# Performance work log

Hardware: AMD Instinct MI355X
Metric: run time of the kernel (lower is better)

The kernel has to match this reference:

```python
import jax, jax.numpy as jnp
import numpy as np
import math

L_DEG, N_PTS, T_ER, P_RAD, C_IN, C_OUT = 4, 8192, 15, 5, 16, 16


def _cg(j1, m1, j2, m2, j3, m3):
    # Clebsch-Gordan coefficient <j1 m1 j2 m2 | j3 m3> (Racah formula),
    # replacing sympy's CG(...).doit() used by the original module.
    if m1 + m2 != m3:
        return 0.0
    if j3 < abs(j1 - j2) or j3 > j1 + j2:
        return 0.0
    f = math.factorial
    pre = math.sqrt((2 * j3 + 1) * f(j3 + j1 - j2) * f(j3 - j1 + j2) * f(j1 + j2 - j3) / f(j1 + j2 + j3 + 1))
    pre *= math.sqrt(f(j3 + m3) * f(j3 - m3) * f(j1 - m1) * f(j1 + m1) * f(j2 - m2) * f(j2 + m2))
    s = 0.0
    for k in range(max(0, j2 - j3 - m1, j1 - j3 + m2), min(j1 + j2 - j3, j1 - m1, j2 + m2) + 1):
        s += (-1.0) ** k / (f(k) * f(j1 + j2 - j3 - k) * f(j1 - m1 - k) * f(j2 + m2 - k) * f(j3 - j2 + m1 + k) * f(j3 - j1 - m2 + k))
    return pre * s


def _precompute(L):
    # Mirrors PrecomputingTensorsForConv6D.
    tens, coefs = [], []
    for l in range(L):
        for l1 in range(L):
            for l2 in range(abs(l - l1), min(L, l + l1 + 1)):
                coefs.append(8.0 * np.pi ** 2 / (2 * l1 + 1)
                             * np.sqrt((2 * l + 1) * (2 * l1 + 1) / (4.0 * np.pi * (2 * l2 + 1)))
                             * _cg(l, 0, l1, 0, l2, 0))
                T1 = np.zeros((l + 1, l1 + 1, l2 + 1), np.float32)
                T2 = np.zeros_like(T1)
                T3 = np.zeros_like(T1)
                for k in range(l + 1):
                    for k1 in range(l1 + 1):
                        if k + k1 < l2 + 1:
                            T1[k, k1, k + k1] = _cg(l, k, l1, k1, l2, k + k1) * (-1) ** k1
                        if k1 > 0 and abs(k - k1) < l2 + 1:
                            if k - k1 >= 0:
                                T2[k, k1, k - k1] = _cg(l, k, l1, -k1, l2, k - k1) * (-1) ** l1
                            else:
                                T3[k, k1, k1 - k] = (-1) ** (k1 - k) * (-1) ** (l1 + l2) * _cg(l, k, l1, -k1, l2, k - k1)
                tens += [T1, T2, T3]
    return tens, [float(c) for c in coefs]


_TENS_NP, _COEFS = _precompute(L_DEG)
_TENS = [jnp.asarray(t, jnp.float32) for t in _TENS_NP]


def _forward(xs, ws, bs):
    L = L_DEG
    # zero the imaginary k=0 rows, as done via temp_term in build()
    ws_m = list(ws)
    bs_m = list(bs)
    for l in range(L):
        mk = (jnp.arange(l + 1) > 0).astype(jnp.float32)
        ws_m[2 * l + 1] = ws[2 * l + 1] * mk[:, None, None, None, None]
        bs_m[2 * l + 1] = bs[2 * l + 1] * mk[None, :, None, None]
    out = []
    itr = 0
    for l in range(L):
        o_r = 0.0
        o_i = 0.0
        for l1 in range(L):
            wr, wi = ws_m[2 * l1], ws_m[2 * l1 + 1]
            for l2 in range(abs(l - l1), min(L, l + l1 + 1)):
                c = _COEFS[itr]
                T1, T2, T3 = _TENS[3 * itr], _TENS[3 * itr + 1], _TENS[3 * itr + 2]
                xr, xi = xs[2 * l2], xs[2 * l2 + 1]
                # x: [n, t, k(l2+1), p, i]; w: [m(l1+1), t, p, i, j]; T: [l(l+1), m, k]
                o_r = o_r + c * jnp.einsum('lmk,ntkpi,mtpij->nlpj', T1 + T2 + T3, xr, wr) \
                          - c * jnp.einsum('lmk,ntkpi,mtpij->nlpj', T1 - T2 + T3, xi, wi)
                o_i = o_i + c * jnp.einsum('lmk,ntkpi,mtpij->nlpj', T1 - T2 - T3, xr, wi) \
                          + c * jnp.einsum('lmk,ntkpi,mtpij->nlpj', T1 + T2 - T3, xi, wr)
                itr += 1
        out.append(o_r + bs_m[2 * l])
        out.append(o_i + bs_m[2 * l + 1])
    return tuple(out)


def setup_inputs() -> dict:
    key = jax.random.key(0)
    ks = jax.random.split(key, 24)
    inp = {}
    i = 0
    for l in range(L_DEG):
        for part in ('r', 'i'):
            inp['x%d%s' % (l, part)] = jax.random.normal(ks[i], (N_PTS, T_ER, l + 1, P_RAD, C_IN), jnp.float32)
            i += 1
    for l in range(L_DEG):
        for part in ('r', 'i'):
            inp['w%d%s' % (l, part)] = jax.random.normal(ks[i], (l + 1, T_ER, P_RAD, C_IN, C_OUT), jnp.float32) * 0.05
            i += 1
    for l in range(L_DEG):
        for part in ('r', 'i'):
            inp['b%d%s' % (l, part)] = jax.random.normal(ks[i], (1, l + 1, P_RAD, C_OUT), jnp.float32) * 0.05
            i += 1
    return inp


def reference(x0r, x0i, x1r, x1i, x2r, x2i, x3r, x3i,
              w0r, w0i, w1r, w1i, w2r, w2i, w3r, w3i,
              b0r, b0i, b1r, b1i, b2r, b2i, b3r, b3i):
    xs = [x0r, x0i, x1r, x1i, x2r, x2i, x3r, x3i]
    ws = [w0r, w0i, w1r, w1i, w2r, w2i, w3r, w3i]
    bs = [b0r, b0i, b1r, b1i, b2r, b2i, b3r, b3i]
    return _forward(xs, ws, bs)
```

## Files before the change

kernel.cpp:

```cpp
#include <hip/hip_runtime.h>

#define PI_D 3.14159265358979323846


typedef __attribute__((ext_vector_type(8))) short short8;
typedef __attribute__((ext_vector_type(4))) float f32x4;

struct Ptrs8 { const float* p[8]; };

__device__ __forceinline__ ushort f2bf(float x){
  uint u = __float_as_uint(x);
  return (ushort)((u + 0x7fffu + ((u>>16)&1u)) >> 16);
}

__device__ __forceinline__ double dfact(int n){ double r=1.0; for(int i=2;i<=n;++i) r*=(double)i; return r; }

__device__ double cg_coef(int j1,int m1,int j2,int m2,int j3,int m3){
  if(m1+m2!=m3) return 0.0;
  if(j3<abs(j1-j2)||j3>j1+j2) return 0.0;
  if(abs(m1)>j1||abs(m2)>j2||abs(m3)>j3) return 0.0;
  double pre = sqrt((2.0*j3+1.0)*dfact(j3+j1-j2)*dfact(j3-j1+j2)*dfact(j1+j2-j3)/dfact(j1+j2+j3+1));
  pre *= sqrt(dfact(j3+m3)*dfact(j3-m3)*dfact(j1-m1)*dfact(j1+m1)*dfact(j2-m2)*dfact(j2+m2));
  int kmin = max(0,max(j2-j3-m1,j1-j3+m2));
  int kmax = min(j1+j2-j3,min(j1-m1,j2+m2));
  double s=0.0;
  for(int k=kmin;k<=kmax;++k){
    double d = dfact(k)*dfact(j1+j2-j3-k)*dfact(j1-m1-k)*dfact(j2+m2-k)*dfact(j3-j2+m1+k)*dfact(j3-j1-m2+k);
    s += ((k&1)?-1.0:1.0)/d;
  }
  return pre*s;
}

__device__ __forceinline__ int gidx(int l,int l2,int combo,int lr,int kx,int l1,int m){
  return ((((((l*4+l2)*4+combo)*4+lr)*4+kx)*4+l1)*4+m);
}

__global__ void g_kernel(float* __restrict__ G){
  int tid = threadIdx.x;
  for(int e=tid;e<16384;e+=blockDim.x) G[e]=0.0f;
  __syncthreads();
  int trip = tid >> 4;
  int sub  = tid & 15;
  int lr = sub >> 2, m = sub & 3;
  int idx=0;
  for(int l=0;l<4;l++)for(int l1=0;l1<4;l1++){
    int lo=abs(l-l1), hi=min(3,l+l1);
    for(int l2=lo;l2<=hi;l2++){
      if(idx==trip && lr<=l && m<=l1){
        double c = 8.0*PI_D*PI_D/(2.0*l1+1.0)
                 * sqrt((2.0*l+1.0)*(2.0*l1+1.0)/(4.0*PI_D*(2.0*l2+1.0)))
                 * cg_coef(l,0,l1,0,l2,0);
        if(lr+m<=l2){
          float f = (float)(c * cg_coef(l,lr,l1,m,l2,lr+m) * ((m&1)?-1.0:1.0));
          G[gidx(l,l2,0,lr,lr+m,l1,m)] += f;
          G[gidx(l,l2,1,lr,lr+m,l1,m)] -= f;
          G[gidx(l,l2,2,lr,lr+m,l1,m)] += f;
          G[gidx(l,l2,3,lr,lr+m,l1,m)] += f;
        }
        if(m>0 && abs(lr-m)<=l2){
          if(lr-m>=0){
            float f = (float)(c * cg_coef(l,lr,l1,-m,l2,lr-m) * ((l1&1)?-1.0:1.0));
            G[gidx(l,l2,0,lr,lr-m,l1,m)] += f;
            G[gidx(l,l2,1,lr,lr-m,l1,m)] += f;
            G[gidx(l,l2,2,lr,lr-m,l1,m)] -= f;
            G[gidx(l,l2,3,lr,lr-m,l1,m)] += f;
          } else {
            float f = (float)(c * (((m-lr)&1)?-1.0:1.0) * (((l1+l2)&1)?-1.0:1.0)
                              * cg_coef(l,lr,l1,-m,l2,lr-m));
            G[gidx(l,l2,0,lr,m-lr,l1,m)] += f;
            G[gidx(l,l2,1,lr,m-lr,l1,m)] -= f;
            G[gidx(l,l2,2,lr,m-lr,l1,m)] -= f;
            G[gidx(l,l2,3,lr,m-lr,l1,m)] -= f;
          }
        }
      }
      idx++;
    }
  }
}

__device__ __forceinline__ void decode_kb(int kb,int& l2,int& partp,int& kx,int& t){
  int kbo;
  if(kb<30){l2=0;kbo=0;} else if(kb<90){l2=1;kbo=30;} else if(kb<180){l2=2;kbo=90;} else {l2=3;kbo=180;}
  int rem = kb-kbo;
  int per = (l2+1)*15;
  partp = rem/per;
  int q = rem%per;
  kx = q/15; t = q%15;
}

__device__ __forceinline__ void decode_col(int col,int& l,int& part,int& lr,int& j){
  int co;
  if(col<32){l=0;co=0;} else if(col<96){l=1;co=32;} else if(col<192){l=2;co=96;} else {l=3;co=192;}
  int cr = col-co; int per=(l+1)*16;
  part = cr/per; int q = cr%per; lr = q>>4; j = q&15;
}

__global__ void w2_kernel(const float* __restrict__ G, Ptrs8 wp, ushort* __restrict__ W2){
  long e = (long)blockIdx.x*256 + threadIdx.x;
  if(e >= 7680000L) return;
  int b8 = (int)(e & 7);
  int ln = (int)((e>>3) & 63);
  int ks = (int)((e>>9) & 1);
  int kt = (int)((e>>10) % 75);
  long rr = (e>>10) / 75;
  int cw = (int)(rr % 20);
  int p  = (int)(rr / 20);
  int col = cw*16 + (ln&15);
  int K = kt*64 + ks*32 + ((ln>>4)<<3) + b8;
  int i = K & 15; int kb = K >> 4;
  int l2,partp,kx,t; decode_kb(kb,l2,partp,kx,t);
  int l,part,lr,j; decode_col(col,l,part,lr,j);
  int combo = (part==0) ? (partp==0?0:1) : (partp==0?2:3);
  int wpart = (combo==0||combo==3)?0:1;
  int mstart = wpart?1:0;
  int woff = t*1280 + p*256 + i*16 + j;
  float acc=0.f;
  for(int l1=0;l1<4;l1++){
    const float* wptr = wp.p[l1*2+wpart];
    int gb = ((((l*4+l2)*4+combo)*4+lr)*4+kx)*16 + l1*4;
    for(int m=mstart;m<=l1;m++){
      float g = G[gb+m];
      if(g!=0.f) acc += g * wptr[m*19200 + woff];
    }
  }
  W2[e] = f2bf(acc);
}

__global__ __launch_bounds__(512) void pack_kernel(Ptrs8 xp, char* __restrict__ Xp5){
  __shared__ ushort L[24000];
  const int tid = threadIdx.x;
  const int n = (blockIdx.x & 7)*1024 + (blockIdx.x >> 3);
  #pragma unroll
  for(int a=0;a<8;a++){
    const int l2 = a>>1, partp = a&1;
    const int kbo = (l2==0)?0:(l2==1)?30:(l2==2)?90:180;
    const int kbase = kbo + partp*15*(l2+1);
    const float* row = xp.p[a] + (long)n*1200*(l2+1);
    const int nf4 = 300*(l2+1);
    for(int u=tid; u<nf4; u+=512){
      float4 v = ((const float4*)row)[u];
      int f = u*4;
      int i = f & 15;
      int r = f >> 4;
      int p = r % 5;
      int tk = r / 5;
      int kx = tk % (l2+1);
      int t  = tk / (l2+1);
      int K = (kbase + kx*15 + t)*16 + i;
      uint2 d;
      d.x = (uint)f2bf(v.x) | ((uint)f2bf(v.y)<<16);
      d.y = (uint)f2bf(v.z) | ((uint)f2bf(v.w)<<16);
      *(uint2*)(&L[p*4800 + K]) = d;
    }
  }
  __syncthreads();
  const int nb = n>>6, rloc = n&63, sw = n&7;
  for(int u=tid; u<3000; u+=512){
    int kt = u/40, rem = u%40;
    int p = rem>>3, c8 = rem&7;
    const uint4 s = *(const uint4*)(&L[p*4800 + kt*64 + c8*8]);
    long off = ((long)(p*128 + nb)*75 + kt)*8192 + rloc*128 + ((c8 ^ sw)<<4);
    *(uint4*)(Xp5 + off) = s;
  }
}


__device__ __forceinline__ void b_load2(const ushort* Wt,int lane,int kt,short8* b){
  #pragma unroll
  for(int ni=0;ni<5;++ni)
    #pragma unroll
    for(int ks=0;ks<2;++ks)
      b[ks*5+ni] = *(const short8*)(Wt + (long)ni*76800 + kt*1024 + ks*512 + lane*8);
}

__device__ __forceinline__ void do_mfma_f(const ushort* A,int lane,const short8* b,f32x4 acc[4][5]){
  #pragma unroll
  for(int ks=0;ks<2;++ks){
    short8 af[4];
    #pragma unroll
    for(int mi=0;mi<4;++mi){
      int row = mi*16 + (lane&15);
      int kc = ks*4 + (lane>>4);
      af[mi] = *(const short8*)(A + row*64 + ((kc ^ (row&7))<<3));
    }
    #pragma unroll
    for(int mi=0;mi<4;++mi)
      #pragma unroll
      for(int ni=0;ni<5;++ni)
        acc[mi][ni] = __builtin_amdgcn_mfma_f32_16x16x32_bf16(af[mi], b[ks*5+ni], acc[mi][ni], 0,0,0);
  }
}

__global__ __launch_bounds__(256,2) void gemm_f(const char* __restrict__ Xp5,
                                                const ushort* __restrict__ W2,
                                                Ptrs8 bp, float* __restrict__ out){
  __shared__ ushort As[2][4096];
  const int tid = threadIdx.x;
  const int lane = tid & 63;
  const int w = tid >> 6;
  int orig = blockIdx.x;
  int xcd = orig & 7, q = orig >> 3;
  const int p = q / 16;
  const int nb = xcd*16 + (q % 16);
  const int n0 = nb*64;
  const char* At = Xp5 + ((long)(p*128 + nb)*75)*8192;
  const ushort* Wt = W2 + (long)(p*20 + w*5)*76800;

  f32x4 acc[4][5] = {};
  uint4 sA0, sA1;
  short8 bfr[10];

  sA0 = *(const uint4*)(At + tid*16);
  sA1 = *(const uint4*)(At + 4096 + tid*16);
  *(uint4*)(&As[0][tid*8]) = sA0;
  *(uint4*)(&As[0][2048 + tid*8]) = sA1;
  b_load2(Wt, lane, 0, bfr);
  __syncthreads();

  int buf = 0;
  #pragma unroll 1
  for(int kt=0;kt<74;++kt){
    sA0 = *(const uint4*)(At + (kt+1)*8192 + tid*16);
    sA1 = *(const uint4*)(At + (kt+1)*8192 + 4096 + tid*16);
    do_mfma_f(&As[buf][0], lane, bfr, acc);
    b_load2(Wt, lane, kt+1, bfr);
    *(uint4*)(&As[buf^1][tid*8]) = sA0;
    *(uint4*)(&As[buf^1][2048 + tid*8]) = sA1;
    __syncthreads();
    buf ^= 1;
  }
  do_mfma_f(&As[buf][0], lane, bfr, acc);

  int j = lane & 15, rg = (lane>>4)*4;
  #pragma unroll
  for(int ni=0;ni<5;++ni){
    int col16 = w*5 + ni;
    int l, part, lr;
    if(col16<2){l=0;part=col16;lr=0;}
    else if(col16<6){int c=col16-2;l=1;part=c>>1;lr=c&1;}
    else if(col16<12){int c=col16-6;l=2;part=(c>=3);lr=part?(c-3):c;}
    else {int c=col16-12;l=3;part=c>>2;lr=c&3;}
    float bv = 0.f;
    if(!(part==1 && lr==0)) bv = bp.p[l*2+part][lr*80 + p*16 + j];
    long base = 655360L*(l+1)*(l+part);
    int nst = (l+1)*80;
    long ioff = base + lr*80 + p*16 + j;
    #pragma unroll
    for(int mi=0;mi<4;++mi){
      int n = n0 + mi*16 + rg;
      #pragma unroll
      for(int r=0;r<4;++r)
        out[ioff + (long)(n+r)*nst] = acc[mi][ni][r] + bv;
    }
  }
}

__device__ __forceinline__ void a_load(const Ptrs8& xp, int p, int n0, int kt, int w, int lane, float4* v){
  int kb = kt*4 + w;
  int l2,partp,kx,t; decode_kb(kb,l2,partp,kx,t);
  const float* xb = xp.p[l2*2+partp];
  int nstr = 1200*(l2+1);
  const float* base = xb + (long)(n0 + (lane>>2))*nstr + (t*(l2+1)+kx)*80 + p*16 + (lane&3)*4;
  long step = (long)16*nstr;
  #pragma unroll
  for(int s=0;s<4;++s) v[s] = *(const float4*)(base + s*step);
}

__device__ __forceinline__ void a_store(ushort* As, int w, int lane, const float4* v){
  int rsub = lane>>2, c4 = (lane&3)*4;
  #pragma unroll
  for(int s=0;s<4;++s){
    int row = s*16 + rsub;
    int e = row*64 + ((w*16 + c4) ^ ((row&7)<<3));
    uint2 d;
    d.x = (uint)f2bf(v[s].x) | ((uint)f2bf(v[s].y)<<16);
    d.y = (uint)f2bf(v[s].z) | ((uint)f2bf(v[s].w)<<16);
    *(uint2*)(As + e) = d;
  }
}

__device__ __forceinline__ void do_mfma64(const ushort* As, int lane, const short8* b, f32x4 acc[4][5]){
  #pragma unroll
  for(int ks=0;ks<2;++ks){
    short8 af[4];
    #pragma unroll
    for(int mi=0;mi<4;++mi){
      int row = mi*16 + (lane&15);
      int e = row*64 + (((ks*32) + (lane>>4)*8) ^ ((row&7)<<3));
      af[mi] = *(const short8*)(As + e);
    }
    #pragma unroll
    for(int mi=0;mi<4;++mi)
      #pragma unroll
      for(int ni=0;ni<5;++ni)
        acc[mi][ni] = __builtin_amdgcn_mfma_f32_16x16x32_bf16(af[mi], b[ks*5+ni], acc[mi][ni], 0,0,0);
  }
}

__global__ __launch_bounds__(256,2) void gemm_direct(Ptrs8 xp, const ushort* __restrict__ W2,
                                                     Ptrs8 bp, float* __restrict__ out){
  __shared__ ushort As[2][4096];
  const int tid = threadIdx.x;
  const int lane = tid & 63;
  const int w = tid >> 6;
  int orig = blockIdx.x;
  int x = orig & 7, q = orig >> 3;
  const int p = q % 5;
  const int nb = (q/5)*8 + x;
  const int n0 = nb*64;
  const ushort* Wt = W2 + (long)(p*20 + w*5)*76800;

  f32x4 acc[4][5] = {};
  float4 av[4];
  short8 bfr[10];

  a_load(xp, p, n0, 0, w, lane, av);
  a_store(&As[0][0], w, lane, av);
  b_load2(Wt, lane, 0, bfr);
  __syncthreads();

  int buf = 0;
  #pragma unroll 1
  for(int kt=0;kt<74;++kt){
    a_load(xp, p, n0, kt+1, w, lane, av);
    do_mfma64(&As[buf][0], lane, bfr, acc);
    b_load2(Wt, lane, kt+1, bfr);
    a_store(&As[buf^1][0], w, lane, av);
    __syncthreads();
    buf ^= 1;
  }
  do_mfma64(&As[buf][0], lane, bfr, acc);

  int j = lane & 15, rg = (lane>>4)*4;
  #pragma unroll
  for(int ni=0;ni<5;++ni){
    int col16 = w*5 + ni;
    int l, part, lr;
    if(col16<2){l=0;part=col16;lr=0;}
    else if(col16<6){int c=col16-2;l=1;part=c>>1;lr=c&1;}
    else if(col16<12){int c=col16-6;l=2;part=(c>=3);lr=part?(c-3):c;}
    else {int c=col16-12;l=3;part=c>>2;lr=c&3;}
    float bv = 0.f;
    if(!(part==1 && lr==0)) bv = bp.p[l*2+part][lr*80 + p*16 + j];
    long base = 655360L*(l+1)*(l+part);
    int nst = (l+1)*80;
    long ioff = base + lr*80 + p*16 + j;
    #pragma unroll
    for(int mi=0;mi<4;++mi){
      int n = n0 + mi*16 + rg;
      #pragma unroll
      for(int r=0;r<4;++r)
        out[ioff + (long)(n+r)*nst] = acc[mi][ni][r] + bv;
    }
  }
}

extern "C" void kernel_launch(void* const* d_in, const int* in_sizes, int n_in,
                              void* d_out, int out_size, void* d_ws, size_t ws_size,
                              hipStream_t stream){
  Ptrs8 xp, wp, bp;
  for(int i=0;i<8;i++){
    xp.p[i] = (const float*)d_in[i];
    wp.p[i] = (const float*)d_in[8+i];
    bp.p[i] = (const float*)d_in[16+i];
  }
  float* G = (float*)d_ws;
  ushort* W2 = (ushort*)((char*)d_ws + 65536);
  g_kernel<<<dim3(1), dim3(576), 0, stream>>>(G);
  w2_kernel<<<dim3(30000), dim3(256), 0, stream>>>(G, wp, W2);
  const size_t need = 16777216ull + 393216000ull;
  if(ws_size >= need){
    char* Xp5 = (char*)d_ws + 16777216;
    pack_kernel<<<dim3(8192), dim3(512), 0, stream>>>(xp, Xp5);
    gemm_f<<<dim3(640), dim3(256), 0, stream>>>(Xp5, W2, bp, (float*)d_out);
  } else {
    gemm_direct<<<dim3(640), dim3(256), 0, stream>>>(xp, W2, bp, (float*)d_out);
  }
}
```

Baseline: 516.2 us.

## Restructure pack kernel to tile by 64-row block and k-tile group

Replaces the per-point pack kernel, which used 8192 blocks each staging one point's full K dimension in shared memory, with 640 blocks that each handle 64 points across 15 k-tiles. A small table of per-k-block base pointers and strides is built in shared memory, each k-tile is staged through a padded LDS tile, and whole 8KB swizzled output tiles are written contiguously. The aim is coalesced, full-tile writes and less LDS per block, at the cost of more scattered global reads and two barriers per k-tile.

```diff
diff --git a/kernel.cpp b/kernel.cpp
--- a/kernel.cpp
+++ b/kernel.cpp
@@ -127,44 +127,53 @@
   W2[e] = f2bf(acc);
 }
 
-__global__ __launch_bounds__(512) void pack_kernel(Ptrs8 xp, char* __restrict__ Xp5){
-  __shared__ ushort L[24000];
+__global__ __launch_bounds__(512,3) void pack_nb(Ptrs8 xp, char* __restrict__ Xp5){
+  __shared__ ushort L[21760];
+  __shared__ int4 KTB[300];
   const int tid = threadIdx.x;
-  const int n = (blockIdx.x & 7)*1024 + (blockIdx.x >> 3);
-  #pragma unroll
-  for(int a=0;a<8;a++){
-    const int l2 = a>>1, partp = a&1;
-    const int kbo = (l2==0)?0:(l2==1)?30:(l2==2)?90:180;
-    const int kbase = kbo + partp*15*(l2+1);
-    const float* row = xp.p[a] + (long)n*1200*(l2+1);
-    const int nf4 = 300*(l2+1);
-    for(int u=tid; u<nf4; u+=512){
-      float4 v = ((const float4*)row)[u];
-      int f = u*4;
-      int i = f & 15;
-      int r = f >> 4;
-      int p = r % 5;
-      int tk = r / 5;
-      int kx = tk % (l2+1);
-      int t  = tk / (l2+1);
-      int K = (kbase + kx*15 + t)*16 + i;
+  const int nb  = blockIdx.x & 127;
+  const int ktg = blockIdx.x >> 7;
+  const int n0 = nb*64;
+
+  for(int e=tid; e<300; e+=512){
+    int l2,partp,kx,t; decode_kb(e,l2,partp,kx,t);
+    const float* bptr = xp.p[l2*2+partp];
+    KTB[e] = make_int4((int)(uint)(unsigned long long)bptr,
+                       (int)((unsigned long long)bptr>>32),
+                       ((t*(l2+1)+kx)*80)*4, (1200*(l2+1))*4);
+  }
+  __syncthreads();
+
+  #pragma unroll 1
+  for(int ktl=0; ktl<15; ++ktl){
+    const int kt = ktg*15 + ktl;
+    #pragma unroll
+    for(int c=0;c<10;++c){
+      int g = c*512 + tid;
+      int row = g/80; int q = g - row*80;
+      int kb_l = q/20; int r20 = q - kb_l*20;
+      int p = r20>>2, i4 = r20&3;
+      int4 tb = KTB[kt*4 + kb_l];
+      const char* src = (const char*)(((unsigned long long)(uint)tb.x) |
+                                      ((unsigned long long)(uint)tb.y<<32))
+                      + (long)(n0+row)*tb.w + tb.z + p*64 + i4*16;
+      float4 v = *(const float4*)src;
       uint2 d;
       d.x = (uint)f2bf(v.x) | ((uint)f2bf(v.y)<<16);
       d.y = (uint)f2bf(v.z) | ((uint)f2bf(v.w)<<16);
-      *(uint2*)(&L[p*4800 + K]) = d;
-    }
-  }
-  __syncthreads();
-  const int nb = n>>6, rloc = n&63, sw = n&7;
-  for(int u=tid; u<3000; u+=512){
-    int kt = u/40, rem = u%40;
-    int p = rem>>3, c8 = rem&7;
-    const uint4 s = *(const uint4*)(&L[p*4800 + kt*64 + c8*8]);
-    long off = ((long)(p*128 + nb)*75 + kt)*8192 + rloc*128 + ((c8 ^ sw)<<4);
-    *(uint4*)(Xp5 + off) = s;
-  }
-}
-
+      *(uint2*)((char*)L + row*680 + p*136 + kb_l*32 + i4*8) = d;
+    }
+    __syncthreads();
+    #pragma unroll
+    for(int c=0;c<5;++c){
+      int g = c*512 + tid;
+      int p = g>>9, rem = g&511, row = rem>>3, c8 = rem&7;
+      uint4 s = *(const uint4*)((const char*)L + row*680 + p*136 + c8*16);
+      *(uint4*)(Xp5 + ((long)(p*128+nb)*75 + kt)*8192 + row*128 + ((c8 ^ (row&7))<<4)) = s;
+    }
+    __syncthreads();
+  }
+}
 
 __device__ __forceinline__ void b_load2(const ushort* Wt,int lane,int kt,short8* b){
   #pragma unroll
@@ -372,7 +381,7 @@
   const size_t need = 16777216ull + 393216000ull;
   if(ws_size >= need){
     char* Xp5 = (char*)d_ws + 16777216;
-    pack_kernel<<<dim3(8192), dim3(512), 0, stream>>>(xp, Xp5);
+    pack_nb<<<dim3(640), dim3(512), 0, stream>>>(xp, Xp5);
     gemm_f<<<dim3(640), dim3(256), 0, stream>>>(Xp5, W2, bp, (float*)d_out);
   } else {
     gemm_direct<<<dim3(640), dim3(256), 0, stream>>>(xp, W2, bp, (float*)d_out);
```

New measurement: 552.1 us. +7.0%, slower.
